# Kernel optimization log

Hardware: AMD Instinct MI355X
Metric: run time of the kernel (lower is better)

## Reference

```python
import jax, jax.numpy as jnp
import numpy as np

EPS = 1e-5

def setup_inputs() -> dict:
    key = jax.random.key(0)
    k1, k2, k3 = jax.random.split(key, 3)
    B, C, H, W = 16, 256, 96, 96
    x = jax.random.normal(k1, (B, C, H, W), dtype=jnp.float32)
    ln_w = jnp.ones((C,), dtype=jnp.float32)
    ln_b = jnp.zeros((C,), dtype=jnp.float32)
    # 1x1 conv weights == dense matrices over channel dim; scaled init
    w_qkv = jax.random.normal(k2, (3 * C, C), dtype=jnp.float32) * (1.0 / np.sqrt(C))
    w_proj = jax.random.normal(k3, (C, C), dtype=jnp.float32) * (1.0 / np.sqrt(C))
    b_proj = jnp.zeros((C,), dtype=jnp.float32)
    return {"x": x, "ln_w": ln_w, "ln_b": ln_b, "w_qkv": w_qkv,
            "w_proj": w_proj, "b_proj": b_proj, "num_heads": 8}

def reference(x, ln_w, ln_b, w_qkv, w_proj, b_proj, num_heads):
    B, C, H, W = x.shape
    n = H * W
    h = num_heads
    d = C // h
    scale = d ** (-0.5)
    xf = x.reshape(B, C, n)  # [B, C, HW]
    # LayerNorm over channel axis (original normalizes x_flat [B,HW,C] on last dim)
    mu = jnp.mean(xf, axis=1, keepdims=True)
    var = jnp.var(xf, axis=1, keepdims=True)
    xn = (xf - mu) * jax.lax.rsqrt(var + EPS) * ln_w[None, :, None] + ln_b[None, :, None]
    # 1x1 conv -> QKV: [B, 3C, HW]
    qkv = jnp.einsum('oc,bcn->bon', w_qkv, xn)
    qkv = qkv.reshape(B, 3, h, d, n)
    q, k, v = qkv[:, 0], qkv[:, 1], qkv[:, 2]  # each [B, h, d, HW]
    # transposed (channel) attention: scores over head-channel dims [B, h, d, d]
    attn = jax.nn.softmax(jnp.einsum('bhdn,bhen->bhde', q, k) * scale, axis=-1)
    xa = jnp.einsum('bhde,bhen->bhdn', attn, v).reshape(B, C, n)
    # proj 1x1 conv + bias
    xp = jnp.einsum('oc,bcn->bon', w_proj, xa) + b_proj[None, :, None]
    # global spatial mean then sigmoid -> [B, C, 1, 1]
    attn_map = jax.nn.sigmoid(jnp.mean(xp, axis=-1))
    return attn_map[:, :, None, None]
```

## Files before the change

### kernel.cpp

```cpp
#include <hip/hip_runtime.h>
#include <hip/hip_bf16.h>

#define NTOT 9216

using short8 = __attribute__((ext_vector_type(8))) short;
using f32x16 = __attribute__((ext_vector_type(16))) float;

__device__ __forceinline__ unsigned short bf16u(float f) {
  __hip_bfloat16 h = __float2bfloat16(f);
  return *reinterpret_cast<unsigned short*>(&h);
}
__device__ __forceinline__ float4 shfl_xor4(float4 v, int m) {
  float4 r;
  r.x = __shfl_xor(v.x, m); r.y = __shfl_xor(v.y, m);
  r.z = __shfl_xor(v.z, m); r.w = __shfl_xor(v.w, m);
  return r;
}

#define TB(buf, r, byte) ((buf) * 36992 + (r) * 144 + (byte))

__global__ __launch_bounds__(1024) void kG(
    const float* __restrict__ x, const float* __restrict__ ln_w,
    const float* __restrict__ ln_b, float* __restrict__ Spart,
    float* __restrict__ xbarp) {
  __shared__ char tile[2 * 36992];
  __shared__ float4 sred1[256], sred2[256];
  __shared__ float lw_s[256], lb_s[256];

  const int t = threadIdx.x, lane = t & 63, w = t >> 6;
  const int colq = t & 15, rowg = t >> 4;
  const int l31 = lane & 31, hi = lane >> 5;
  const int wr = w >> 2, wc = w & 3;
  const int b = blockIdx.x >> 4, p = blockIdx.x & 15;
  const float* xb = x + (size_t)b * 256 * NTOT;

  if (t < 256) { lw_s[t] = ln_w[t]; lb_s[t] = ln_b[t]; }

  f32x16 acc[2][2];
#pragma unroll
  for (int m = 0; m < 2; ++m)
#pragma unroll
    for (int n = 0; n < 2; ++n)
#pragma unroll
      for (int r = 0; r < 16; ++r) acc[m][n][r] = 0.f;
  float xacc[4] = {0.f, 0.f, 0.f, 0.f};

  int n0 = p * 9 * 64;
  float4 vreg[4];
#pragma unroll
  for (int j = 0; j < 4; ++j)
    vreg[j] = *reinterpret_cast<const float4*>(xb + (size_t)(rowg + 64 * j) * NTOT + n0 + colq * 4);

  for (int i = 0; i < 9; ++i) {
    const int buf = i & 1;
    float4 s1 = {0.f, 0.f, 0.f, 0.f}, s2 = {0.f, 0.f, 0.f, 0.f};
#pragma unroll
    for (int j = 0; j < 4; ++j) {
      const float4 v = vreg[j];
      s1.x += v.x; s1.y += v.y; s1.z += v.z; s1.w += v.w;
      s2.x += v.x * v.x; s2.y += v.y * v.y; s2.z += v.z * v.z; s2.w += v.w * v.w;
    }
    s1 += shfl_xor4(s1, 16); s1 += shfl_xor4(s1, 32);
    s2 += shfl_xor4(s2, 16); s2 += shfl_xor4(s2, 32);
    if (lane < 16) { sred1[w * 16 + lane] = s1; sred2[w * 16 + lane] = s2; }
    __syncthreads();
    {
      float4 a1 = {0.f, 0.f, 0.f, 0.f}, a2 = {0.f, 0.f, 0.f, 0.f};
#pragma unroll
      for (int ww = 0; ww < 16; ++ww) {
        float4 u1 = sred1[ww * 16 + colq], u2 = sred2[ww * 16 + colq];
        a1.x += u1.x; a1.y += u1.y; a1.z += u1.z; a1.w += u1.w;
        a2.x += u2.x; a2.y += u2.y; a2.z += u2.z; a2.w += u2.w;
      }
      const float inv = 1.f / 256.f;
      float4 mu, rc;
      mu.x = a1.x * inv; mu.y = a1.y * inv; mu.z = a1.z * inv; mu.w = a1.w * inv;
      rc.x = rsqrtf(a2.x * inv - mu.x * mu.x + 1e-5f);
      rc.y = rsqrtf(a2.y * inv - mu.y * mu.y + 1e-5f);
      rc.z = rsqrtf(a2.z * inv - mu.z * mu.z + 1e-5f);
      rc.w = rsqrtf(a2.w * inv - mu.w * mu.w + 1e-5f);
#pragma unroll
      for (int j = 0; j < 4; ++j) {
        const int r = rowg + 64 * j;
        const float g = lw_s[r], bb = lb_s[r];
        float f0 = (vreg[j].x - mu.x) * rc.x * g + bb;
        float f1 = (vreg[j].y - mu.y) * rc.y * g + bb;
        float f2 = (vreg[j].z - mu.z) * rc.z * g + bb;
        float f3 = (vreg[j].w - mu.w) * rc.w * g + bb;
        ushort4 o;
        o.x = bf16u(f0); o.y = bf16u(f1); o.z = bf16u(f2); o.w = bf16u(f3);
        *reinterpret_cast<ushort4*>(tile + TB(buf, r, colq * 8)) = o;
        xacc[j] += f0 + f1 + f2 + f3;
      }
    }
    if (i < 8) {
      const int n1 = n0 + 64;
#pragma unroll
      for (int j = 0; j < 4; ++j)
        vreg[j] = *reinterpret_cast<const float4*>(xb + (size_t)(rowg + 64 * j) * NTOT + n1 + colq * 4);
    }
    __syncthreads();
#pragma unroll
    for (int kk = 0; kk < 4; ++kk) {
      short8 a0 = *reinterpret_cast<short8*>(tile + TB(buf, wr * 64 + l31,      kk * 32 + hi * 16));
      short8 a1 = *reinterpret_cast<short8*>(tile + TB(buf, wr * 64 + 32 + l31, kk * 32 + hi * 16));
      short8 b0 = *reinterpret_cast<short8*>(tile + TB(buf, wc * 64 + l31,      kk * 32 + hi * 16));
      short8 b1 = *reinterpret_cast<short8*>(tile + TB(buf, wc * 64 + 32 + l31, kk * 32 + hi * 16));
      acc[0][0] = __builtin_amdgcn_mfma_f32_32x32x16_bf16(a0, b0, acc[0][0], 0, 0, 0);
      acc[0][1] = __builtin_amdgcn_mfma_f32_32x32x16_bf16(a0, b1, acc[0][1], 0, 0, 0);
      acc[1][0] = __builtin_amdgcn_mfma_f32_32x32x16_bf16(a1, b0, acc[1][0], 0, 0, 0);
      acc[1][1] = __builtin_amdgcn_mfma_f32_32x32x16_bf16(a1, b1, acc[1][1], 0, 0, 0);
    }
    n0 += 64;
  }

  float* Sp = Spart + (size_t)blockIdx.x * 65536;
#pragma unroll
  for (int m = 0; m < 2; ++m)
#pragma unroll
    for (int n = 0; n < 2; ++n)
#pragma unroll
      for (int r = 0; r < 16; ++r) {
        const int row = wr * 64 + m * 32 + (r & 3) + 8 * (r >> 2) + 4 * hi;
        const int col = wc * 64 + n * 32 + l31;
        Sp[row * 256 + col] = acc[m][n][r];
      }
#pragma unroll
  for (int j = 0; j < 4; ++j) {
    float s = xacc[j];
    s += __shfl_xor(s, 1); s += __shfl_xor(s, 2);
    s += __shfl_xor(s, 4); s += __shfl_xor(s, 8);
    if ((lane & 15) == 0) xbarp[blockIdx.x * 256 + 64 * j + rowg] = s;
  }
}

__global__ __launch_bounds__(256) void kR(const float4* __restrict__ Spart,
                                          float4* __restrict__ S) {
  const int idx = blockIdx.x * 256 + threadIdx.x;
  const int b = idx >> 14, o = idx & 16383;
  float4 a = {0.f, 0.f, 0.f, 0.f};
#pragma unroll
  for (int p = 0; p < 16; ++p) {
    float4 v = Spart[(size_t)(b * 16 + p) * 16384 + o];
    a.x += v.x; a.y += v.y; a.z += v.z; a.w += v.w;
  }
  S[(size_t)b * 16384 + o] = a;
}

__global__ __launch_bounds__(256) void kC2(const float* __restrict__ S,
    const float* __restrict__ w_qkv, const float* __restrict__ xbarp,
    float* __restrict__ xabar) {
  __shared__ float wq_s[32 * 257];
  __shared__ float wk_s[32 * 257];
  __shared__ float att[32 * 33];
  __shared__ float xnb[256], vbp[256], vbar[32];
  const int t = threadIdx.x;
  const int b = blockIdx.x >> 3, h = blockIdx.x & 7;
  const float* Wq = w_qkv + (size_t)(h * 32) * 256;
  const float* Wk = w_qkv + (size_t)(256 + h * 32) * 256;
  const float* Wv = w_qkv + (size_t)(512 + h * 32) * 256;
  for (int i = t; i < 8192; i += 256) {
    const int r = i >> 8, c = i & 255;
    wq_s[r * 257 + c] = Wq[i];
    wk_s[r * 257 + c] = Wk[i];
  }
  {
    float s = 0.f;
#pragma unroll
    for (int p = 0; p < 16; ++p) s += xbarp[(b * 16 + p) * 256 + t];
    xnb[t] = s * (1.f / (float)NTOT);
  }
  __syncthreads();
  {
    const int e = t & 31, seg = t >> 5;
    float s = 0.f;
#pragma unroll
    for (int cc = 0; cc < 32; ++cc)
      s += Wv[e * 256 + seg * 32 + cc] * xnb[seg * 32 + cc];
    vbp[seg * 32 + e] = s;
  }
  __syncthreads();
  if (t < 32) {
    float s = 0.f;
#pragma unroll
    for (int seg = 0; seg < 8; ++seg) s += vbp[seg * 32 + t];
    vbar[t] = s;
  }
  float acc[32];
#pragma unroll
  for (int d = 0; d < 32; ++d) acc[d] = 0.f;
  const float* Sb = S + (size_t)b * 65536;
  for (int c = 0; c < 256; ++c) {
    const float sv = Sb[c * 256 + t];
#pragma unroll
    for (int d = 0; d < 32; ++d) acc[d] += wq_s[d * 257 + c] * sv;
  }
  __syncthreads();
#pragma unroll
  for (int d = 0; d < 32; ++d) wq_s[d * 257 + t] = acc[d];
  __syncthreads();
  {
    const int d = t >> 3, e0 = (t & 7) * 4;
    float l0 = 0.f, l1 = 0.f, l2 = 0.f, l3 = 0.f;
    for (int c = 0; c < 256; ++c) {
      const float tv = wq_s[d * 257 + c];
      l0 += tv * wk_s[(e0 + 0) * 257 + c];
      l1 += tv * wk_s[(e0 + 1) * 257 + c];
      l2 += tv * wk_s[(e0 + 2) * 257 + c];
      l3 += tv * wk_s[(e0 + 3) * 257 + c];
    }
    const float scale = 0.17677669529663687f;
    att[d * 33 + e0 + 0] = l0 * scale;
    att[d * 33 + e0 + 1] = l1 * scale;
    att[d * 33 + e0 + 2] = l2 * scale;
    att[d * 33 + e0 + 3] = l3 * scale;
  }
  __syncthreads();
  if (t < 32) {
    float mx = -1e30f;
#pragma unroll
    for (int e = 0; e < 32; ++e) mx = fmaxf(mx, att[t * 33 + e]);
    float sm = 0.f, xa = 0.f;
#pragma unroll
    for (int e = 0; e < 32; ++e) {
      float pe = expf(att[t * 33 + e] - mx);
      sm += pe; xa += pe * vbar[e];
    }
    xabar[b * 256 + h * 32 + t] = xa / sm;
  }
}

__global__ __launch_bounds__(256) void kD_out(const float* __restrict__ xabar,
    const float* __restrict__ w_proj, const float* __restrict__ b_proj,
    float* __restrict__ out) {
  __shared__ float xa[256];
  const int t = threadIdx.x, b = blockIdx.x;
  xa[t] = xabar[b * 256 + t];
  __syncthreads();
  float acc = b_proj[t];
  const float4* wp = reinterpret_cast<const float4*>(w_proj + (size_t)t * 256);
  const float4* xav = reinterpret_cast<const float4*>(xa);
#pragma unroll 4
  for (int c = 0; c < 64; ++c) {
    float4 wv = wp[c], xv = xav[c];
    acc += wv.x * xv.x + wv.y * xv.y + wv.z * xv.z + wv.w * xv.w;
  }
  out[b * 256 + t] = 1.f / (1.f + expf(-acc));
}

extern "C" void kernel_launch(void* const* d_in, const int* in_sizes, int n_in,
                              void* d_out, int out_size, void* d_ws, size_t ws_size,
                              hipStream_t stream) {
  const float* x      = (const float*)d_in[0];
  const float* ln_w   = (const float*)d_in[1];
  const float* ln_b   = (const float*)d_in[2];
  const float* w_qkv  = (const float*)d_in[3];
  const float* w_proj = (const float*)d_in[4];
  const float* b_proj = (const float*)d_in[5];
  float* out = (float*)d_out;

  char* ws = (char*)d_ws;
  float* Spart = (float*)ws;
  float* xbarp = (float*)(ws + 67108864);
  float* S     = (float*)(ws + 67371008);
  float* xabar = (float*)(ws + 71565312);

  kG<<<256, 1024, 0, stream>>>(x, ln_w, ln_b, Spart, xbarp);
  kR<<<1024, 256, 0, stream>>>((const float4*)Spart, (float4*)S);
  kC2<<<128, 256, 0, stream>>>(S, w_qkv, xbarp, xabar);
  kD_out<<<16, 256, 0, stream>>>(xabar, w_proj, b_proj, out);
}
```

Baseline: 315.7 us.

## Split Gram kernel into half-row blocks of 512 threads for higher occupancy

The LayerNorm plus Gram-matrix kernel now launches 512 blocks of 512 threads instead of 256 blocks of 1024. Each pair of blocks loads the same x tile and computes half of the 256x256 output rows. The register prefetch and the double-buffered LDS tile are removed. Raw x is staged as bf16 in a single LDS tile and normalized in place from those bf16 values. The aim is more resident blocks per CU and lower LDS use, at the cost of reading x twice (hopefully served from cache) and doing LayerNorm on bf16-rounded inputs, which loses precision.

```diff
diff --git a/kernel.cpp b/kernel.cpp
--- a/kernel.cpp
+++ b/kernel.cpp
@@ -9,6 +9,10 @@
 __device__ __forceinline__ unsigned short bf16u(float f) {
   __hip_bfloat16 h = __float2bfloat16(f);
   return *reinterpret_cast<unsigned short*>(&h);
+}
+__device__ __forceinline__ float bf16f(unsigned short u) {
+  unsigned int x = ((unsigned int)u) << 16;
+  return __uint_as_float(x);
 }
 __device__ __forceinline__ float4 shfl_xor4(float4 v, int m) {
   float4 r;
@@ -17,21 +21,23 @@
   return r;
 }
 
-#define TB(buf, r, byte) ((buf) * 36992 + (r) * 144 + (byte))
-
-__global__ __launch_bounds__(1024) void kG(
+#define TB(r, byte) ((r) * 144 + (byte))
+
+__global__ __launch_bounds__(512, 4) void kG(
     const float* __restrict__ x, const float* __restrict__ ln_w,
     const float* __restrict__ ln_b, float* __restrict__ Spart,
     float* __restrict__ xbarp) {
-  __shared__ char tile[2 * 36992];
-  __shared__ float4 sred1[256], sred2[256];
+  __shared__ char tile[36864];
+  __shared__ float4 sred1[128], sred2[128];
   __shared__ float lw_s[256], lb_s[256];
 
   const int t = threadIdx.x, lane = t & 63, w = t >> 6;
   const int colq = t & 15, rowg = t >> 4;
   const int l31 = lane & 31, hi = lane >> 5;
-  const int wr = w >> 2, wc = w & 3;
-  const int b = blockIdx.x >> 4, p = blockIdx.x & 15;
+  const int bp = blockIdx.x >> 1;
+  const int half = blockIdx.x & 1;
+  const int b = bp >> 4, p = bp & 15;
+  const int wr = half * 2 + (w >> 2), wc = w & 3;
   const float* xb = x + (size_t)b * 256 * NTOT;
 
   if (t < 256) { lw_s[t] = ln_w[t]; lb_s[t] = ln_b[t]; }
@@ -43,78 +49,73 @@
     for (int n = 0; n < 2; ++n)
 #pragma unroll
       for (int r = 0; r < 16; ++r) acc[m][n][r] = 0.f;
-  float xacc[4] = {0.f, 0.f, 0.f, 0.f};
-
-  int n0 = p * 9 * 64;
-  float4 vreg[4];
-#pragma unroll
-  for (int j = 0; j < 4; ++j)
-    vreg[j] = *reinterpret_cast<const float4*>(xb + (size_t)(rowg + 64 * j) * NTOT + n0 + colq * 4);
-
+  float xsum[8];
+#pragma unroll
+  for (int j = 0; j < 8; ++j) xsum[j] = 0.f;
+
+  int n0 = p * 576;
   for (int i = 0; i < 9; ++i) {
-    const int buf = i & 1;
+    if (i) __syncthreads();
+    const float* xp = xb + n0 + colq * 4;
     float4 s1 = {0.f, 0.f, 0.f, 0.f}, s2 = {0.f, 0.f, 0.f, 0.f};
 #pragma unroll
-    for (int j = 0; j < 4; ++j) {
-      const float4 v = vreg[j];
+    for (int j = 0; j < 8; ++j) {
+      const int r = rowg + 32 * j;
+      float4 v = *reinterpret_cast<const float4*>(xp + (size_t)r * NTOT);
       s1.x += v.x; s1.y += v.y; s1.z += v.z; s1.w += v.w;
       s2.x += v.x * v.x; s2.y += v.y * v.y; s2.z += v.z * v.z; s2.w += v.w * v.w;
+      ushort4 u;
+      u.x = bf16u(v.x); u.y = bf16u(v.y); u.z = bf16u(v.z); u.w = bf16u(v.w);
+      *reinterpret_cast<ushort4*>(tile + TB(r, colq * 8)) = u;
     }
     s1 += shfl_xor4(s1, 16); s1 += shfl_xor4(s1, 32);
     s2 += shfl_xor4(s2, 16); s2 += shfl_xor4(s2, 32);
     if (lane < 16) { sred1[w * 16 + lane] = s1; sred2[w * 16 + lane] = s2; }
     __syncthreads();
-    {
-      float4 a1 = {0.f, 0.f, 0.f, 0.f}, a2 = {0.f, 0.f, 0.f, 0.f};
-#pragma unroll
-      for (int ww = 0; ww < 16; ++ww) {
-        float4 u1 = sred1[ww * 16 + colq], u2 = sred2[ww * 16 + colq];
-        a1.x += u1.x; a1.y += u1.y; a1.z += u1.z; a1.w += u1.w;
-        a2.x += u2.x; a2.y += u2.y; a2.z += u2.z; a2.w += u2.w;
-      }
-      const float inv = 1.f / 256.f;
-      float4 mu, rc;
-      mu.x = a1.x * inv; mu.y = a1.y * inv; mu.z = a1.z * inv; mu.w = a1.w * inv;
-      rc.x = rsqrtf(a2.x * inv - mu.x * mu.x + 1e-5f);
-      rc.y = rsqrtf(a2.y * inv - mu.y * mu.y + 1e-5f);
-      rc.z = rsqrtf(a2.z * inv - mu.z * mu.z + 1e-5f);
-      rc.w = rsqrtf(a2.w * inv - mu.w * mu.w + 1e-5f);
-#pragma unroll
-      for (int j = 0; j < 4; ++j) {
-        const int r = rowg + 64 * j;
-        const float g = lw_s[r], bb = lb_s[r];
-        float f0 = (vreg[j].x - mu.x) * rc.x * g + bb;
-        float f1 = (vreg[j].y - mu.y) * rc.y * g + bb;
-        float f2 = (vreg[j].z - mu.z) * rc.z * g + bb;
-        float f3 = (vreg[j].w - mu.w) * rc.w * g + bb;
-        ushort4 o;
-        o.x = bf16u(f0); o.y = bf16u(f1); o.z = bf16u(f2); o.w = bf16u(f3);
-        *reinterpret_cast<ushort4*>(tile + TB(buf, r, colq * 8)) = o;
-        xacc[j] += f0 + f1 + f2 + f3;
-      }
-    }
-    if (i < 8) {
-      const int n1 = n0 + 64;
-#pragma unroll
-      for (int j = 0; j < 4; ++j)
-        vreg[j] = *reinterpret_cast<const float4*>(xb + (size_t)(rowg + 64 * j) * NTOT + n1 + colq * 4);
+    float4 a1 = {0.f, 0.f, 0.f, 0.f}, a2 = {0.f, 0.f, 0.f, 0.f};
+#pragma unroll
+    for (int ww = 0; ww < 8; ++ww) {
+      float4 u1 = sred1[ww * 16 + colq], u2 = sred2[ww * 16 + colq];
+      a1.x += u1.x; a1.y += u1.y; a1.z += u1.z; a1.w += u1.w;
+      a2.x += u2.x; a2.y += u2.y; a2.z += u2.z; a2.w += u2.w;
+    }
+    const float inv = 1.f / 256.f;
+    float4 mu, rc;
+    mu.x = a1.x * inv; mu.y = a1.y * inv; mu.z = a1.z * inv; mu.w = a1.w * inv;
+    rc.x = rsqrtf(a2.x * inv - mu.x * mu.x + 1e-5f);
+    rc.y = rsqrtf(a2.y * inv - mu.y * mu.y + 1e-5f);
+    rc.z = rsqrtf(a2.z * inv - mu.z * mu.z + 1e-5f);
+    rc.w = rsqrtf(a2.w * inv - mu.w * mu.w + 1e-5f);
+#pragma unroll
+    for (int j = 0; j < 8; ++j) {
+      const int r = rowg + 32 * j;
+      ushort4 u = *reinterpret_cast<ushort4*>(tile + TB(r, colq * 8));
+      const float g = lw_s[r], bb = lb_s[r];
+      float f0 = (bf16f(u.x) - mu.x) * rc.x * g + bb;
+      float f1 = (bf16f(u.y) - mu.y) * rc.y * g + bb;
+      float f2 = (bf16f(u.z) - mu.z) * rc.z * g + bb;
+      float f3 = (bf16f(u.w) - mu.w) * rc.w * g + bb;
+      ushort4 o;
+      o.x = bf16u(f0); o.y = bf16u(f1); o.z = bf16u(f2); o.w = bf16u(f3);
+      *reinterpret_cast<ushort4*>(tile + TB(r, colq * 8)) = o;
+      xsum[j] += f0 + f1 + f2 + f3;
     }
     __syncthreads();
 #pragma unroll
     for (int kk = 0; kk < 4; ++kk) {
-      short8 a0 = *reinterpret_cast<short8*>(tile + TB(buf, wr * 64 + l31,      kk * 32 + hi * 16));
-      short8 a1 = *reinterpret_cast<short8*>(tile + TB(buf, wr * 64 + 32 + l31, kk * 32 + hi * 16));
-      short8 b0 = *reinterpret_cast<short8*>(tile + TB(buf, wc * 64 + l31,      kk * 32 + hi * 16));
-      short8 b1 = *reinterpret_cast<short8*>(tile + TB(buf, wc * 64 + 32 + l31, kk * 32 + hi * 16));
+      short8 a0 = *reinterpret_cast<short8*>(tile + TB(wr * 64 + l31,      kk * 32 + hi * 16));
+      short8 a1v = *reinterpret_cast<short8*>(tile + TB(wr * 64 + 32 + l31, kk * 32 + hi * 16));
+      short8 b0 = *reinterpret_cast<short8*>(tile + TB(wc * 64 + l31,      kk * 32 + hi * 16));
+      short8 b1 = *reinterpret_cast<short8*>(tile + TB(wc * 64 + 32 + l31, kk * 32 + hi * 16));
       acc[0][0] = __builtin_amdgcn_mfma_f32_32x32x16_bf16(a0, b0, acc[0][0], 0, 0, 0);
       acc[0][1] = __builtin_amdgcn_mfma_f32_32x32x16_bf16(a0, b1, acc[0][1], 0, 0, 0);
-      acc[1][0] = __builtin_amdgcn_mfma_f32_32x32x16_bf16(a1, b0, acc[1][0], 0, 0, 0);
-      acc[1][1] = __builtin_amdgcn_mfma_f32_32x32x16_bf16(a1, b1, acc[1][1], 0, 0, 0);
+      acc[1][0] = __builtin_amdgcn_mfma_f32_32x32x16_bf16(a1v, b0, acc[1][0], 0, 0, 0);
+      acc[1][1] = __builtin_amdgcn_mfma_f32_32x32x16_bf16(a1v, b1, acc[1][1], 0, 0, 0);
     }
     n0 += 64;
   }
 
-  float* Sp = Spart + (size_t)blockIdx.x * 65536;
+  float* Sp = Spart + (size_t)bp * 65536;
 #pragma unroll
   for (int m = 0; m < 2; ++m)
 #pragma unroll
@@ -126,11 +127,12 @@
         Sp[row * 256 + col] = acc[m][n][r];
       }
 #pragma unroll
-  for (int j = 0; j < 4; ++j) {
-    float s = xacc[j];
+  for (int j = 0; j < 8; ++j) {
+    float s = xsum[j];
     s += __shfl_xor(s, 1); s += __shfl_xor(s, 2);
     s += __shfl_xor(s, 4); s += __shfl_xor(s, 8);
-    if ((lane & 15) == 0) xbarp[blockIdx.x * 256 + 64 * j + rowg] = s;
+    if ((lane & 15) == 0 && half == (j >> 2))
+      xbarp[bp * 256 + rowg + 32 * j] = s;
   }
 }
 
@@ -265,7 +267,7 @@
   float* S     = (float*)(ws + 67371008);
   float* xabar = (float*)(ws + 71565312);
 
-  kG<<<256, 1024, 0, stream>>>(x, ln_w, ln_b, Spart, xbarp);
+  kG<<<512, 512, 0, stream>>>(x, ln_w, ln_b, Spart, xbarp);
   kR<<<1024, 256, 0, stream>>>((const float4*)Spart, (float4*)S);
   kC2<<<128, 256, 0, stream>>>(S, w_qkv, xbarp, xabar);
   kD_out<<<16, 256, 0, stream>>>(xabar, w_proj, b_proj, out);
```

Measured after the change: 346.8 us. 9.8% more time.

## Software-pipeline LayerNorm stats and MFMA Gram across a three-slot LDS ring

Applied to the files above, without the earlier changes.

Restructures the main loop so each iteration stages raw x as bf16 into a three-slot shared tile ring and computes partial stats for tile i. Normalization and the MFMA Gram accumulation for tile i-1 happen in the same iteration, behind one barrier instead of two. The goal is to remove a barrier per iteration and overlap the global loads and reductions with matrix work. In exchange it uses more LDS, adds an extra shared-memory read/write pass, and normalizes from bf16-rounded inputs rather than fp32 values, which lowers accuracy.

```diff
diff --git a/kernel.cpp b/kernel.cpp
--- a/kernel.cpp
+++ b/kernel.cpp
@@ -9,6 +9,10 @@
 __device__ __forceinline__ unsigned short bf16u(float f) {
   __hip_bfloat16 h = __float2bfloat16(f);
   return *reinterpret_cast<unsigned short*>(&h);
+}
+__device__ __forceinline__ float bf16f(unsigned short u) {
+  unsigned int x = ((unsigned int)u) << 16;
+  return __uint_as_float(x);
 }
 __device__ __forceinline__ float4 shfl_xor4(float4 v, int m) {
   float4 r;
@@ -17,14 +21,21 @@
   return r;
 }
 
-#define TB(buf, r, byte) ((buf) * 36992 + (r) * 144 + (byte))
+#define TB(slot, r, byte) ((slot) * 36992 + (r) * 144 + (byte))
+
+#define PIPE_SYNC()                                      \
+  do {                                                   \
+    asm volatile("s_waitcnt lgkmcnt(0)" ::: "memory");   \
+    __builtin_amdgcn_s_barrier();                        \
+    __builtin_amdgcn_sched_barrier(0);                   \
+  } while (0)
 
 __global__ __launch_bounds__(1024) void kG(
     const float* __restrict__ x, const float* __restrict__ ln_w,
     const float* __restrict__ ln_b, float* __restrict__ Spart,
     float* __restrict__ xbarp) {
-  __shared__ char tile[2 * 36992];
-  __shared__ float4 sred1[256], sred2[256];
+  __shared__ char tile[3 * 36992];
+  __shared__ float4 sred1[2][256], sred2[2][256];
   __shared__ float lw_s[256], lb_s[256];
 
   const int t = threadIdx.x, lane = t & 63, w = t >> 6;
@@ -45,30 +56,45 @@
       for (int r = 0; r < 16; ++r) acc[m][n][r] = 0.f;
   float xacc[4] = {0.f, 0.f, 0.f, 0.f};
 
-  int n0 = p * 9 * 64;
   float4 vreg[4];
-#pragma unroll
-  for (int j = 0; j < 4; ++j)
-    vreg[j] = *reinterpret_cast<const float4*>(xb + (size_t)(rowg + 64 * j) * NTOT + n0 + colq * 4);
-
-  for (int i = 0; i < 9; ++i) {
-    const int buf = i & 1;
-    float4 s1 = {0.f, 0.f, 0.f, 0.f}, s2 = {0.f, 0.f, 0.f, 0.f};
-#pragma unroll
-    for (int j = 0; j < 4; ++j) {
-      const float4 v = vreg[j];
-      s1.x += v.x; s1.y += v.y; s1.z += v.z; s1.w += v.w;
-      s2.x += v.x * v.x; s2.y += v.y * v.y; s2.z += v.z * v.z; s2.w += v.w * v.w;
-    }
-    s1 += shfl_xor4(s1, 16); s1 += shfl_xor4(s1, 32);
-    s2 += shfl_xor4(s2, 16); s2 += shfl_xor4(s2, 32);
-    if (lane < 16) { sred1[w * 16 + lane] = s1; sred2[w * 16 + lane] = s2; }
-    __syncthreads();
-    {
+  {
+    const float* xp = xb + p * 576 + colq * 4;
+#pragma unroll
+    for (int j = 0; j < 4; ++j)
+      vreg[j] = *reinterpret_cast<const float4*>(xp + (size_t)(rowg + 64 * j) * NTOT);
+  }
+
+  int cur = 0;
+  for (int i = 0; i <= 9; ++i) {
+    const int prevslot = (cur + 2) % 3;
+    if (i <= 8) {
+      const int sb = i & 1;
+      float4 s1 = {0.f, 0.f, 0.f, 0.f}, s2 = {0.f, 0.f, 0.f, 0.f};
+#pragma unroll
+      for (int j = 0; j < 4; ++j) {
+        const float4 v = vreg[j];
+        s1.x += v.x; s1.y += v.y; s1.z += v.z; s1.w += v.w;
+        s2.x += v.x * v.x; s2.y += v.y * v.y; s2.z += v.z * v.z; s2.w += v.w * v.w;
+        ushort4 u;
+        u.x = bf16u(v.x); u.y = bf16u(v.y); u.z = bf16u(v.z); u.w = bf16u(v.w);
+        *reinterpret_cast<ushort4*>(tile + TB(cur, rowg + 64 * j, colq * 8)) = u;
+      }
+      s1 += shfl_xor4(s1, 16); s1 += shfl_xor4(s1, 32);
+      s2 += shfl_xor4(s2, 16); s2 += shfl_xor4(s2, 32);
+      if (lane < 16) { sred1[sb][w * 16 + lane] = s1; sred2[sb][w * 16 + lane] = s2; }
+    }
+    if (i <= 7) {
+      const float* xp = xb + p * 576 + (i + 1) * 64 + colq * 4;
+#pragma unroll
+      for (int j = 0; j < 4; ++j)
+        vreg[j] = *reinterpret_cast<const float4*>(xp + (size_t)(rowg + 64 * j) * NTOT);
+    }
+    if (i >= 1) {
+      const int sb = (i - 1) & 1;
       float4 a1 = {0.f, 0.f, 0.f, 0.f}, a2 = {0.f, 0.f, 0.f, 0.f};
 #pragma unroll
       for (int ww = 0; ww < 16; ++ww) {
-        float4 u1 = sred1[ww * 16 + colq], u2 = sred2[ww * 16 + colq];
+        float4 u1 = sred1[sb][ww * 16 + colq], u2 = sred2[sb][ww * 16 + colq];
         a1.x += u1.x; a1.y += u1.y; a1.z += u1.z; a1.w += u1.w;
         a2.x += u2.x; a2.y += u2.y; a2.z += u2.z; a2.w += u2.w;
       }
@@ -82,36 +108,33 @@
 #pragma unroll
       for (int j = 0; j < 4; ++j) {
         const int r = rowg + 64 * j;
+        ushort4 u = *reinterpret_cast<ushort4*>(tile + TB(prevslot, r, colq * 8));
         const float g = lw_s[r], bb = lb_s[r];
-        float f0 = (vreg[j].x - mu.x) * rc.x * g + bb;
-        float f1 = (vreg[j].y - mu.y) * rc.y * g + bb;
-        float f2 = (vreg[j].z - mu.z) * rc.z * g + bb;
-        float f3 = (vreg[j].w - mu.w) * rc.w * g + bb;
+        float f0 = (bf16f(u.x) - mu.x) * rc.x * g + bb;
+        float f1 = (bf16f(u.y) - mu.y) * rc.y * g + bb;
+        float f2 = (bf16f(u.z) - mu.z) * rc.z * g + bb;
+        float f3 = (bf16f(u.w) - mu.w) * rc.w * g + bb;
         ushort4 o;
         o.x = bf16u(f0); o.y = bf16u(f1); o.z = bf16u(f2); o.w = bf16u(f3);
-        *reinterpret_cast<ushort4*>(tile + TB(buf, r, colq * 8)) = o;
+        *reinterpret_cast<ushort4*>(tile + TB(prevslot, r, colq * 8)) = o;
         xacc[j] += f0 + f1 + f2 + f3;
       }
     }
-    if (i < 8) {
-      const int n1 = n0 + 64;
-#pragma unroll
-      for (int j = 0; j < 4; ++j)
-        vreg[j] = *reinterpret_cast<const float4*>(xb + (size_t)(rowg + 64 * j) * NTOT + n1 + colq * 4);
-    }
-    __syncthreads();
-#pragma unroll
-    for (int kk = 0; kk < 4; ++kk) {
-      short8 a0 = *reinterpret_cast<short8*>(tile + TB(buf, wr * 64 + l31,      kk * 32 + hi * 16));
-      short8 a1 = *reinterpret_cast<short8*>(tile + TB(buf, wr * 64 + 32 + l31, kk * 32 + hi * 16));
-      short8 b0 = *reinterpret_cast<short8*>(tile + TB(buf, wc * 64 + l31,      kk * 32 + hi * 16));
-      short8 b1 = *reinterpret_cast<short8*>(tile + TB(buf, wc * 64 + 32 + l31, kk * 32 + hi * 16));
-      acc[0][0] = __builtin_amdgcn_mfma_f32_32x32x16_bf16(a0, b0, acc[0][0], 0, 0, 0);
-      acc[0][1] = __builtin_amdgcn_mfma_f32_32x32x16_bf16(a0, b1, acc[0][1], 0, 0, 0);
-      acc[1][0] = __builtin_amdgcn_mfma_f32_32x32x16_bf16(a1, b0, acc[1][0], 0, 0, 0);
-      acc[1][1] = __builtin_amdgcn_mfma_f32_32x32x16_bf16(a1, b1, acc[1][1], 0, 0, 0);
-    }
-    n0 += 64;
+    PIPE_SYNC();
+    if (i >= 1) {
+#pragma unroll
+      for (int kk = 0; kk < 4; ++kk) {
+        short8 a0 = *reinterpret_cast<short8*>(tile + TB(prevslot, wr * 64 + l31,      kk * 32 + hi * 16));
+        short8 a1v = *reinterpret_cast<short8*>(tile + TB(prevslot, wr * 64 + 32 + l31, kk * 32 + hi * 16));
+        short8 b0 = *reinterpret_cast<short8*>(tile + TB(prevslot, wc * 64 + l31,      kk * 32 + hi * 16));
+        short8 b1 = *reinterpret_cast<short8*>(tile + TB(prevslot, wc * 64 + 32 + l31, kk * 32 + hi * 16));
+        acc[0][0] = __builtin_amdgcn_mfma_f32_32x32x16_bf16(a0, b0, acc[0][0], 0, 0, 0);
+        acc[0][1] = __builtin_amdgcn_mfma_f32_32x32x16_bf16(a0, b1, acc[0][1], 0, 0, 0);
+        acc[1][0] = __builtin_amdgcn_mfma_f32_32x32x16_bf16(a1v, b0, acc[1][0], 0, 0, 0);
+        acc[1][1] = __builtin_amdgcn_mfma_f32_32x32x16_bf16(a1v, b1, acc[1][1], 0, 0, 0);
+      }
+    }
+    cur = (cur == 2) ? 0 : cur + 1;
   }
 
   float* Sp = Spart + (size_t)blockIdx.x * 65536;
```

Measured after the change: 542.1 us. +71.7%, slower.
